# Kernel optimization log

Hardware: AMD Instinct MI355X
Metric: run time of the kernel (lower is better)

## Reference

```python
import jax, jax.numpy as jnp
import numpy as np

DIM_MODEL = 1024
NUM_HEADS = 16
HEAD_DIM = DIM_MODEL // NUM_HEADS
DIM_POS = 64
EVENT_HORIZON = 1e-06
MAX_FORCE = 50.0
CURVATURE = 0.15


def setup_inputs() -> dict:
    key = jax.random.key(0)
    k1, k2, k3, k4 = jax.random.split(key, 4)
    B, S = 2, 2048
    x = jax.random.normal(k1, (B, S, DIM_MODEL), dtype=jnp.float32)
    positions = jax.random.normal(k2, (S, DIM_POS), dtype=jnp.float32)
    # learned params
    W_mass = jax.random.normal(k3, (NUM_HEADS, HEAD_DIM), dtype=jnp.float32) * (1.0 / np.sqrt(HEAD_DIM))
    G = jnp.asarray([1.0 * 0.9 ** h for h in range(NUM_HEADS)], dtype=jnp.float32)
    W_out = jax.random.normal(k4, (DIM_MODEL, DIM_MODEL), dtype=jnp.float32) * (1.0 / np.sqrt(DIM_MODEL))
    return {"x": x, "positions": positions, "W_mass": W_mass, "G": G, "W_out": W_out}


def reference(x, positions, W_mass, G, W_out):
    B, S, D = x.shape
    H, hd = NUM_HEADS, HEAD_DIM
    xh = x.reshape(B, S, H, hd)                      # per-head slices (contiguous split)
    # per-head scalar "mass" per token: softplus(Linear(head_dim -> 1, no bias))
    masses = jax.nn.softplus(jnp.einsum('bshd,hd->bhs', xh, W_mass))  # [B,H,S]
    # shared squared distances between positions, with curvature warp
    diff = positions[None, :, :] - positions[:, None, :]  # [S,S,P]
    dist_sq = jnp.sum(diff * diff, axis=-1)               # [S,S]
    dist_norm = jnp.sqrt(dist_sq + EVENT_HORIZON)
    dist_sq = dist_sq * (1.0 + CURVATURE * jnp.cos(dist_norm))
    dist_sq = jnp.maximum(dist_sq, EVENT_HORIZON)
    # gravitational force scores F_ij = G * m_i * m_j / dist_sq, Hawking-clamped
    Gabs = jnp.abs(G)[None, :, None, None]                # [1,H,1,1]
    forces = Gabs * masses[:, :, :, None] * masses[:, :, None, :] / dist_sq[None, None]
    forces = jnp.minimum(forces, MAX_FORCE)               # [B,H,S,S]
    attn = jax.nn.softmax(forces, axis=-1)
    out = jnp.einsum('bhst,bthd->bshd', attn, xh).reshape(B, S, D)
    return out @ W_out.T
```

## Files before the change

### kernel.cpp

```cpp
#include <hip/hip_runtime.h>
#include <hip/hip_bf16.h>

#define SEQ 2048
#define DMODEL 1024
#define NHEAD 16
#define HDIM 64
#define DPOS 64
#define BATCH 2

constexpr float EVENT_HORIZON = 1e-6f;
constexpr float MAX_FORCE = 50.0f;
constexpr float CURV = 0.15f;
constexpr float LOG2E = 1.44269504f;
constexpr float SHIFT = 39.0f;

typedef __attribute__((ext_vector_type(8))) short frag8;
typedef __attribute__((ext_vector_type(4))) unsigned int uint4v;
typedef __attribute__((ext_vector_type(8))) _Float16 half8;
typedef __attribute__((ext_vector_type(2))) _Float16 half2t;
typedef __attribute__((ext_vector_type(4))) float frag4f;

union A8u { half8 v; half2t h[4]; };

__device__ inline short bfbits(float f) {
  __hip_bfloat16 h = __float2bfloat16(f);
  return *reinterpret_cast<short*>(&h);
}
__device__ inline float fbits(unsigned u) {
  union { unsigned u; float f; } c; c.u = u; return c.f;
}
__device__ inline half2t pkrtz(float a, float b) {
  return __builtin_bit_cast(half2t, __builtin_amdgcn_cvt_pkrtz(a, b));
}
__device__ inline float exp2_fast(float x) {
  float r;
  asm("v_exp_f32 %0, %1" : "=v"(r) : "v"(x));
  return r;
}
__device__ inline unsigned pkmax(unsigned a, unsigned b) {
  unsigned d;
  asm("v_pk_max_i16 %0, %1, %2" : "=v"(d) : "v"(a), "v"(b));
  return d;
}
__device__ inline int swz(int row, int u) { return row * 8 + (u ^ (row & 7)); }

__global__ __launch_bounds__(256) void prep_and_dist(
    const float* __restrict__ x, const float* __restrict__ Wm,
    const float* __restrict__ pos, const float* __restrict__ Wout,
    _Float16* __restrict__ xt, float* __restrict__ masses,
    unsigned short* __restrict__ invd, _Float16* __restrict__ wh) {
  __shared__ float Li[64 * 68];
  __shared__ float Lj[64 * 68];
  int bid = blockIdx.x;
  int t = threadIdx.x;

  if (bid >= 3072) {
    int i = (bid - 3072) * 256 + t;
    float4 v = ((const float4*)Wout)[i];
    _Float16 o[4] = {(_Float16)v.x, (_Float16)v.y, (_Float16)v.z, (_Float16)v.w};
    *(float2*)(wh + 4 * (size_t)i) = *(float2*)o;
    return;
  }

  if (bid < 2048) {
    int bh = bid & 31;
    int h = bh & 15, b = bh >> 4;
    int d = t & 63;
    int jg = (t >> 6) + ((bid >> 5) << 2);
    int j0 = jg * 8;
    const float* src = x + (size_t)(b * SEQ) * DMODEL + h * HDIM + d;
    float wmd = Wm[h * HDIM + d];
    half8 v;
    float fv[8];
#pragma unroll
    for (int jj = 0; jj < 8; ++jj) {
      float f = src[(size_t)(j0 + jj) * DMODEL];
      fv[jj] = f;
      v[jj] = (_Float16)f;
    }
    *(half8*)(xt + ((size_t)bh * HDIM + d) * SEQ + j0) = v;

    float msum = 0.f;
#pragma unroll
    for (int jj = 0; jj < 8; ++jj) {
      float s = fv[jj] * wmd;
#pragma unroll
      for (int off = 32; off; off >>= 1) s += __shfl_xor(s, off, 64);
      if (d == jj) msum = s;
    }
    if (d < 8) {
      float m = (msum > 20.f) ? msum : log1pf(expf(msum));
      masses[(size_t)bh * SEQ + j0 + d] = m;
    }
    return;
  }

  int ib = bid - 2048;
  int i0 = (ib >> 5) * 64, j0 = (ib & 31) * 64;
  if (i0 > j0) return;

  int kk = (t & 15) * 4;
  int rr = t >> 4;
#pragma unroll
  for (int q = 0; q < 4; ++q) {
    int row = q * 16 + rr;
    float4 a = *(const float4*)(pos + (size_t)(i0 + row) * DPOS + kk);
    float4 b = *(const float4*)(pos + (size_t)(j0 + row) * DPOS + kk);
    Li[(kk + 0) * 68 + row] = a.x; Li[(kk + 1) * 68 + row] = a.y;
    Li[(kk + 2) * 68 + row] = a.z; Li[(kk + 3) * 68 + row] = a.w;
    Lj[(kk + 0) * 68 + row] = b.x; Lj[(kk + 1) * 68 + row] = b.y;
    Lj[(kk + 2) * 68 + row] = b.z; Lj[(kk + 3) * 68 + row] = b.w;
  }
  __syncthreads();

  int ti = (t >> 4) * 4;
  int tj = (t & 15) * 4;

  float acc[4][4];
#pragma unroll
  for (int a = 0; a < 4; ++a)
#pragma unroll
    for (int b = 0; b < 4; ++b) acc[a][b] = 0.f;

#pragma unroll 8
  for (int k = 0; k < 64; ++k) {
    float4 a = *(const float4*)(&Li[k * 68 + ti]);
    float4 b = *(const float4*)(&Lj[k * 68 + tj]);
    float av[4] = {a.x, a.y, a.z, a.w};
    float bv[4] = {b.x, b.y, b.z, b.w};
#pragma unroll
    for (int mi = 0; mi < 4; ++mi)
#pragma unroll
      for (int mj = 0; mj < 4; ++mj) {
        float d = av[mi] - bv[mj];
        acc[mi][mj] += d * d;
      }
  }

  unsigned short op[4][4];
#pragma unroll
  for (int mi = 0; mi < 4; ++mi) {
#pragma unroll
    for (int mj = 0; mj < 4; ++mj) {
      float d2 = acc[mi][mj];
      float dn = sqrtf(d2 + EVENT_HORIZON);
      float wv = d2 * (1.f + CURV * __cosf(dn));
      op[mi][mj] = (unsigned short)bfbits(1.0f / fmaxf(wv, EVENT_HORIZON));
    }
    ushort4 o = {op[mi][0], op[mi][1], op[mi][2], op[mi][3]};
    *(ushort4*)(&invd[(size_t)(i0 + ti + mi) * SEQ + j0 + tj]) = o;
  }
#pragma unroll
  for (int mj = 0; mj < 4; ++mj) {
    ushort4 o = {op[0][mj], op[1][mj], op[2][mj], op[3][mj]};
    *(ushort4*)(&invd[(size_t)(j0 + tj + mj) * SEQ + i0 + ti]) = o;
  }
}

__global__ __launch_bounds__(256, 4) void attn_mfma_kernel(
    const _Float16* __restrict__ xt, const float* __restrict__ masses,
    const unsigned short* __restrict__ invd, const float* __restrict__ G,
    _Float16* __restrict__ attnout) {
  __shared__ _Float16 Vs[2][2][64 * 64];
  __shared__ float Ms[2][128];
  __shared__ float Mmax[16];

  constexpr float S2 = SHIFT * LOG2E;
  constexpr float C2 = (MAX_FORCE - SHIFT) * LOG2E;
  constexpr float THR = S2 - 26.f;

  int bid = blockIdx.x;
  int bh = (bid & 7) * 4 + ((bid >> 3) & 3);
  int iblk = bid >> 5;
  int h = bh & (NHEAD - 1), b = bh >> 4;
  int i0 = iblk * 64;
  int t = threadIdx.x, w = t >> 6, lane = t & 63;
  int l15 = lane & 15, quad = lane >> 4;
  int iw = i0 + w * 16;

  float gabs = fabsf(G[h]);
  const float* mrow = masses + (size_t)bh * SEQ;
  float cm = gabs * mrow[iw + l15] * LOG2E;
  const unsigned short* ivrow = invd + (size_t)(iw + l15) * SEQ;

  float cmx = cm;
#pragma unroll
  for (int off = 1; off < 16; off <<= 1) cmx = fmaxf(cmx, __shfl_xor(cmx, off, 64));

  int srow = t >> 2, sunit = (t & 3) * 2;
  const _Float16* srcrow =
      xt + ((size_t)bh * HDIM + srow) * SEQ + sunit * 8;
  int swzoff0 = swz(srow, sunit) * 8;
  int swzoff1 = swz(srow, sunit + 1) * 8;

  half8 vone;
#pragma unroll
  for (int k = 0; k < 8; ++k) vone[k] = (_Float16)1.f;

  frag4f acc[4];
#pragma unroll
  for (int nt = 0; nt < 4; ++nt) acc[nt] = (frag4f)0.f;
  frag4f accs = (frag4f)0.f;

  {
    const float* mp = mrow + t * 8;
    float4 q0 = *(const float4*)(mp);
    float4 q1 = *(const float4*)(mp + 4);
    float v0 = fmaxf(fmaxf(fmaxf(q0.x, q0.y), fmaxf(q0.z, q0.w)),
                     fmaxf(fmaxf(q1.x, q1.y), fmaxf(q1.z, q1.w)));
#pragma unroll
    for (int off = 1; off < 16; off <<= 1) v0 = fmaxf(v0, __shfl_xor(v0, off, 64));
    if ((t & 15) == 0) Mmax[t >> 4] = v0;
  }

  *(half8*)(&Vs[0][0][0] + swzoff0) = *(const half8*)(srcrow);
  *(half8*)(&Vs[0][0][0] + swzoff1) = *(const half8*)(srcrow + 8);
  *(half8*)(&Vs[0][1][0] + swzoff0) = *(const half8*)(srcrow + 64);
  *(half8*)(&Vs[0][1][0] + swzoff1) = *(const half8*)(srcrow + 72);
  if (t < 128) Ms[0][t] = mrow[t];
  frag8 iv_cur[4], iv_nxt[4];
  iv_cur[0] = *(const frag8*)(ivrow + quad * 8);
  iv_cur[1] = *(const frag8*)(ivrow + 32 + quad * 8);
  iv_cur[2] = *(const frag8*)(ivrow + 64 + quad * 8);
  iv_cur[3] = *(const frag8*)(ivrow + 96 + quad * 8);
  __syncthreads();

  for (int cc = 0; cc < 8; ++cc) {
#pragma unroll
    for (int u = 0; u < 2; ++u) {
      int c = cc * 2 + u;
      int jn = (c + 1) * 128;
      half8 vpre0, vpre1, vpre2, vpre3;
      float mload = 0.f;

      if (c < 15) {
        vpre0 = *(const half8*)(srcrow + jn);
        vpre1 = *(const half8*)(srcrow + jn + 8);
        if (t < 128) mload = mrow[jn + t];
        iv_nxt[0] = *(const frag8*)(ivrow + jn + quad * 8);
        iv_nxt[1] = *(const frag8*)(ivrow + jn + 32 + quad * 8);
      }

      bool live;
      {
        uint4v q0 = __builtin_bit_cast(uint4v, iv_cur[0]);
        uint4v q1 = __builtin_bit_cast(uint4v, iv_cur[1]);
        uint4v q2 = __builtin_bit_cast(uint4v, iv_cur[2]);
        uint4v q3 = __builtin_bit_cast(uint4v, iv_cur[3]);
        unsigned m0 = pkmax(pkmax(q0[0], q1[0]), pkmax(q2[0], q3[0]));
        unsigned m1 = pkmax(pkmax(q0[1], q1[1]), pkmax(q2[1], q3[1]));
        unsigned m2 = pkmax(pkmax(q0[2], q1[2]), pkmax(q2[2], q3[2]));
        unsigned m3 = pkmax(pkmax(q0[3], q1[3]), pkmax(q2[3], q3[3]));
        unsigned r = pkmax(pkmax(m0, m1), pkmax(m2, m3));
        float ivm = fmaxf(fbits(r << 16), fbits(r & 0xffff0000u));
#pragma unroll
        for (int off = 1; off < 64; off <<= 1)
          ivm = fmaxf(ivm, __shfl_xor(ivm, off, 64));
        live = (cmx * Mmax[c] * ivm >= THR);
      }

      const float* Mbase = &Ms[u][0];
      auto unit = [&](const _Float16* Vb, int sub, int kh, frag8 ivv) {
        const float* mp = Mbase + sub * 64 + kh * 32 + quad * 8;
        float4 mjl = *(const float4*)(mp);
        float4 mjh = *(const float4*)(mp + 4);
        float mjf[8] = {mjl.x, mjl.y, mjl.z, mjl.w,
                        mjh.x, mjh.y, mjh.z, mjh.w};
        uint4v uv = __builtin_bit_cast(uint4v, ivv);
        float e[8];
#pragma unroll
        for (int p = 0; p < 4; ++p) {
          float ivA = fbits(uv[p] << 16);
          float ivB = fbits(uv[p] & 0xffff0000u);
          float fA = fmaf(cm * mjf[2 * p], ivA, -S2);
          float fB = fmaf(cm * mjf[2 * p + 1], ivB, -S2);
          e[2 * p] = exp2_fast(fminf(fA, C2));
          e[2 * p + 1] = exp2_fast(fminf(fB, C2));
        }
        A8u A;
#pragma unroll
        for (int p = 0; p < 4; ++p)
          A.h[p] = pkrtz(e[2 * p], e[2 * p + 1]);

        __builtin_amdgcn_s_setprio(1);
        accs = __builtin_amdgcn_mfma_f32_16x16x32_f16(A.v, vone, accs, 0, 0, 0);
#pragma unroll
        for (int nt = 0; nt < 4; ++nt) {
          half8 Bf = *(const half8*)(Vb + swz(nt * 16 + l15, kh * 4 + quad) * 8);
          acc[nt] = __builtin_amdgcn_mfma_f32_16x16x32_f16(A.v, Bf, acc[nt], 0, 0, 0);
        }
        __builtin_amdgcn_s_setprio(0);
      };

      if (live) {
        unit(&Vs[u][0][0], 0, 0, iv_cur[0]);
        unit(&Vs[u][0][0], 0, 1, iv_cur[1]);
      }

      if (c < 15) {
        vpre2 = *(const half8*)(srcrow + jn + 64);
        vpre3 = *(const half8*)(srcrow + jn + 72);
        iv_nxt[2] = *(const frag8*)(ivrow + jn + 64 + quad * 8);
        iv_nxt[3] = *(const frag8*)(ivrow + jn + 96 + quad * 8);
      }

      if (live) {
        unit(&Vs[u][1][0], 1, 0, iv_cur[2]);
        unit(&Vs[u][1][0], 1, 1, iv_cur[3]);
      }

      if (c < 15) {
        _Float16* Vn = &Vs[u ^ 1][0][0];
        *(half8*)(Vn + swzoff0) = vpre0;
        *(half8*)(Vn + swzoff1) = vpre1;
        *(half8*)(Vn + 4096 + swzoff0) = vpre2;
        *(half8*)(Vn + 4096 + swzoff1) = vpre3;
        if (t < 128) Ms[u ^ 1][t] = mload;
        iv_cur[0] = iv_nxt[0]; iv_cur[1] = iv_nxt[1];
        iv_cur[2] = iv_nxt[2]; iv_cur[3] = iv_nxt[3];
      }
      __syncthreads();
    }
  }

#pragma unroll
  for (int reg = 0; reg < 4; ++reg) {
    int r = quad * 4 + reg;
    float s = 1.f / accs[reg];
#pragma unroll
    for (int nt = 0; nt < 4; ++nt) {
      attnout[(size_t)(b * SEQ + iw + r) * DMODEL + h * HDIM + nt * 16 + l15] =
          (_Float16)(acc[nt][reg] * s);
    }
  }
}

__global__ __launch_bounds__(512, 4) void out_gemm_mfma(
    const _Float16* __restrict__ Ag, const _Float16* __restrict__ Wg,
    float* __restrict__ C) {
  __shared__ _Float16 As[2][128 * 64];
  __shared__ _Float16 Bs[2][64 * 64];

  int bid = blockIdx.x;
  int xcd = bid & 7, local = bid >> 3;
  int m0 = (xcd * 4 + (local >> 4)) * 128;
  int n0 = (local & 15) * 64;

  int t = threadIdx.x, w = t >> 6, lane = t & 63;
  int l15 = lane & 15, quad = lane >> 4;
  int mh = (w >> 1) * 32, nh = (w & 1) * 32;

  int ar = t >> 2;  int au = (t & 3) * 2;
  int br = t >> 3;  int bu = t & 7;
  const _Float16* abase = Ag + (size_t)(m0 + ar) * DMODEL + au * 8;
  const _Float16* wbase = Wg + (size_t)(n0 + br) * DMODEL + bu * 8;

  frag4f acc[2][2];
#pragma unroll
  for (int mt = 0; mt < 2; ++mt)
#pragma unroll
    for (int nt = 0; nt < 2; ++nt) acc[mt][nt] = (frag4f)0.f;

  half8 a0, a1, b0;
  auto loadk = [&](int kc) {
    const _Float16* ap = abase + kc * 64;
    a0 = *(const half8*)(ap);
    a1 = *(const half8*)(ap + 8);
    b0 = *(const half8*)(wbase + kc * 64);
  };
  auto stage = [&](int buf) {
    _Float16* aw = As[buf]; _Float16* bw = Bs[buf];
    *(half8*)(aw + swz(ar, au + 0) * 8) = a0;
    *(half8*)(aw + swz(ar, au + 1) * 8) = a1;
    *(half8*)(bw + swz(br, bu) * 8) = b0;
  };

  loadk(0);
  stage(0);
  __syncthreads();

  for (int kk = 0; kk < 8; ++kk) {
#pragma unroll
    for (int u = 0; u < 2; ++u) {
      int kc = kk * 2 + u;
      if (kc < 15) loadk(kc + 1);

      const _Float16* ac = As[u];
      const _Float16* bc = Bs[u];
#pragma unroll
      for (int kh = 0; kh < 2; ++kh) {
        half8 Af[2], Bf[2];
#pragma unroll
        for (int mt = 0; mt < 2; ++mt)
          Af[mt] = *(const half8*)(ac + swz(mh + mt * 16 + l15, kh * 4 + quad) * 8);
#pragma unroll
        for (int nt = 0; nt < 2; ++nt)
          Bf[nt] = *(const half8*)(bc + swz(nh + nt * 16 + l15, kh * 4 + quad) * 8);
        __builtin_amdgcn_s_setprio(1);
#pragma unroll
        for (int mt = 0; mt < 2; ++mt)
#pragma unroll
          for (int nt = 0; nt < 2; ++nt)
            acc[mt][nt] = __builtin_amdgcn_mfma_f32_16x16x32_f16(Af[mt], Bf[nt], acc[mt][nt], 0, 0, 0);
        __builtin_amdgcn_s_setprio(0);
      }

      if (kc < 15) stage(u ^ 1);
      __syncthreads();
    }
  }

#pragma unroll
  for (int mt = 0; mt < 2; ++mt)
#pragma unroll
    for (int nt = 0; nt < 2; ++nt)
#pragma unroll
      for (int reg = 0; reg < 4; ++reg) {
        int m = m0 + mh + mt * 16 + quad * 4 + reg;
        int n = n0 + nh + nt * 16 + l15;
        C[(size_t)m * DMODEL + n] = acc[mt][nt][reg];
      }
}

extern "C" void kernel_launch(void* const* d_in, const int* in_sizes, int n_in,
                              void* d_out, int out_size, void* d_ws, size_t ws_size,
                              hipStream_t stream) {
  const float* x    = (const float*)d_in[0];
  const float* pos  = (const float*)d_in[1];
  const float* Wm   = (const float*)d_in[2];
  const float* G    = (const float*)d_in[3];
  const float* Wout = (const float*)d_in[4];
  float* out = (float*)d_out;

  char* wsb = (char*)d_ws;
  float* masses = (float*)wsb;
  unsigned short* invd = (unsigned short*)(wsb + (1 << 18));
  _Float16* attnout = (_Float16*)(wsb + (1 << 18) + (8 << 20));
  _Float16* xt      = (_Float16*)(wsb + (1 << 18) + (16 << 20));
  _Float16* wh      = (_Float16*)(wsb + (1 << 18) + (24 << 20));

  prep_and_dist<<<dim3(4096), 256, 0, stream>>>(
      x, Wm, pos, Wout, xt, masses, invd, wh);
  attn_mfma_kernel<<<dim3(1024), 256, 0, stream>>>(
      xt, masses, invd, G, attnout);
  out_gemm_mfma<<<dim3(512), 512, 0, stream>>>(attnout, wh, out);
}
```

Measured before the change: 150.7 us.

## Precompute per-tile inverse-distance maxima and skip loads for dead attention chunks

```diff
diff --git a/kernel.cpp b/kernel.cpp
--- a/kernel.cpp
+++ b/kernel.cpp
@@ -37,18 +37,14 @@
   asm("v_exp_f32 %0, %1" : "=v"(r) : "v"(x));
   return r;
 }
-__device__ inline unsigned pkmax(unsigned a, unsigned b) {
-  unsigned d;
-  asm("v_pk_max_i16 %0, %1, %2" : "=v"(d) : "v"(a), "v"(b));
-  return d;
-}
 __device__ inline int swz(int row, int u) { return row * 8 + (u ^ (row & 7)); }
 
 __global__ __launch_bounds__(256) void prep_and_dist(
     const float* __restrict__ x, const float* __restrict__ Wm,
     const float* __restrict__ pos, const float* __restrict__ Wout,
     _Float16* __restrict__ xt, float* __restrict__ masses,
-    unsigned short* __restrict__ invd, _Float16* __restrict__ wh) {
+    unsigned short* __restrict__ invd, _Float16* __restrict__ wh,
+    float* __restrict__ tilemax) {
   __shared__ float Li[64 * 68];
   __shared__ float Lj[64 * 68];
   int bid = blockIdx.x;
@@ -138,6 +134,7 @@
   }
 
   unsigned short op[4][4];
+  int mloc = 0;
 #pragma unroll
   for (int mi = 0; mi < 4; ++mi) {
 #pragma unroll
@@ -146,6 +143,7 @@
       float dn = sqrtf(d2 + EVENT_HORIZON);
       float wv = d2 * (1.f + CURV * __cosf(dn));
       op[mi][mj] = (unsigned short)bfbits(1.0f / fmaxf(wv, EVENT_HORIZON));
+      mloc = max(mloc, (int)op[mi][mj]);
     }
     ushort4 o = {op[mi][0], op[mi][1], op[mi][2], op[mi][3]};
     *(ushort4*)(&invd[(size_t)(i0 + ti + mi) * SEQ + j0 + tj]) = o;
@@ -155,15 +153,32 @@
     ushort4 o = {op[0][mj], op[1][mj], op[2][mj], op[3][mj]};
     *(ushort4*)(&invd[(size_t)(j0 + tj + mj) * SEQ + i0 + ti]) = o;
   }
+
+#pragma unroll
+  for (int off = 1; off < 64; off <<= 1)
+    mloc = max(mloc, __shfl_xor(mloc, off, 64));
+  __syncthreads();
+  if ((t & 63) == 0) ((int*)Li)[t >> 6] = mloc;
+  __syncthreads();
+  if (t == 0) {
+    int mm = max(max(((int*)Li)[0], ((int*)Li)[1]),
+                 max(((int*)Li)[2], ((int*)Li)[3]));
+    float fm = fbits((unsigned)mm << 16);
+    int it = ib >> 5, jt = ib & 31;
+    tilemax[it * 32 + jt] = fm;
+    tilemax[jt * 32 + it] = fm;
+  }
 }
 
 __global__ __launch_bounds__(256, 4) void attn_mfma_kernel(
     const _Float16* __restrict__ xt, const float* __restrict__ masses,
     const unsigned short* __restrict__ invd, const float* __restrict__ G,
-    _Float16* __restrict__ attnout) {
+    const float* __restrict__ tilemax, _Float16* __restrict__ attnout) {
   __shared__ _Float16 Vs[2][2][64 * 64];
   __shared__ float Ms[2][128];
   __shared__ float Mmax[16];
+  __shared__ float CMW[4];
+  __shared__ int Lv[16];
 
   constexpr float S2 = SHIFT * LOG2E;
   constexpr float C2 = (MAX_FORCE - SHIFT) * LOG2E;
@@ -183,10 +198,6 @@
   float cm = gabs * mrow[iw + l15] * LOG2E;
   const unsigned short* ivrow = invd + (size_t)(iw + l15) * SEQ;
 
-  float cmx = cm;
-#pragma unroll
-  for (int off = 1; off < 16; off <<= 1) cmx = fmaxf(cmx, __shfl_xor(cmx, off, 64));
-
   int srow = t >> 2, sunit = (t & 3) * 2;
   const _Float16* srcrow =
       xt + ((size_t)bh * HDIM + srow) * SEQ + sunit * 8;
@@ -211,6 +222,12 @@
 #pragma unroll
     for (int off = 1; off < 16; off <<= 1) v0 = fmaxf(v0, __shfl_xor(v0, off, 64));
     if ((t & 15) == 0) Mmax[t >> 4] = v0;
+  }
+  {
+    float cmx = cm;
+#pragma unroll
+    for (int off = 1; off < 16; off <<= 1) cmx = fmaxf(cmx, __shfl_xor(cmx, off, 64));
+    if (lane == 0) CMW[w] = cmx;
   }
 
   *(half8*)(&Vs[0][0][0] + swzoff0) = *(const half8*)(srcrow);
@@ -225,38 +242,34 @@
   iv_cur[3] = *(const frag8*)(ivrow + 96 + quad * 8);
   __syncthreads();
 
+  if (t < 16) {
+    float cmb = fmaxf(fmaxf(CMW[0], CMW[1]), fmaxf(CMW[2], CMW[3]));
+    float ivm = fmaxf(tilemax[iblk * 32 + 2 * t], tilemax[iblk * 32 + 2 * t + 1]);
+    Lv[t] = (cmb * Mmax[t] * ivm >= THR) ? 1 : 0;
+  }
+  __syncthreads();
+  unsigned livemask = 0;
+#pragma unroll
+  for (int c2 = 0; c2 < 16; ++c2)
+    livemask |= (unsigned)(Lv[c2] != 0) << c2;
+  livemask = __builtin_amdgcn_readfirstlane(livemask);
+
   for (int cc = 0; cc < 8; ++cc) {
 #pragma unroll
     for (int u = 0; u < 2; ++u) {
       int c = cc * 2 + u;
       int jn = (c + 1) * 128;
+      bool lvc = (livemask >> c) & 1;
+      bool lvn = (c < 15) && ((livemask >> (c + 1)) & 1);
       half8 vpre0, vpre1, vpre2, vpre3;
       float mload = 0.f;
 
-      if (c < 15) {
+      if (lvn) {
         vpre0 = *(const half8*)(srcrow + jn);
         vpre1 = *(const half8*)(srcrow + jn + 8);
         if (t < 128) mload = mrow[jn + t];
         iv_nxt[0] = *(const frag8*)(ivrow + jn + quad * 8);
         iv_nxt[1] = *(const frag8*)(ivrow + jn + 32 + quad * 8);
-      }
-
-      bool live;
-      {
-        uint4v q0 = __builtin_bit_cast(uint4v, iv_cur[0]);
-        uint4v q1 = __builtin_bit_cast(uint4v, iv_cur[1]);
-        uint4v q2 = __builtin_bit_cast(uint4v, iv_cur[2]);
-        uint4v q3 = __builtin_bit_cast(uint4v, iv_cur[3]);
-        unsigned m0 = pkmax(pkmax(q0[0], q1[0]), pkmax(q2[0], q3[0]));
-        unsigned m1 = pkmax(pkmax(q0[1], q1[1]), pkmax(q2[1], q3[1]));
-        unsigned m2 = pkmax(pkmax(q0[2], q1[2]), pkmax(q2[2], q3[2]));
-        unsigned m3 = pkmax(pkmax(q0[3], q1[3]), pkmax(q2[3], q3[3]));
-        unsigned r = pkmax(pkmax(m0, m1), pkmax(m2, m3));
-        float ivm = fmaxf(fbits(r << 16), fbits(r & 0xffff0000u));
-#pragma unroll
-        for (int off = 1; off < 64; off <<= 1)
-          ivm = fmaxf(ivm, __shfl_xor(ivm, off, 64));
-        live = (cmx * Mmax[c] * ivm >= THR);
       }
 
       const float* Mbase = &Ms[u][0];
@@ -292,24 +305,24 @@
         __builtin_amdgcn_s_setprio(0);
       };
 
-      if (live) {
+      if (lvc) {
         unit(&Vs[u][0][0], 0, 0, iv_cur[0]);
         unit(&Vs[u][0][0], 0, 1, iv_cur[1]);
       }
 
-      if (c < 15) {
+      if (lvn) {
         vpre2 = *(const half8*)(srcrow + jn + 64);
         vpre3 = *(const half8*)(srcrow + jn + 72);
         iv_nxt[2] = *(const frag8*)(ivrow + jn + 64 + quad * 8);
         iv_nxt[3] = *(const frag8*)(ivrow + jn + 96 + quad * 8);
       }
 
-      if (live) {
+      if (lvc) {
         unit(&Vs[u][1][0], 1, 0, iv_cur[2]);
         unit(&Vs[u][1][0], 1, 1, iv_cur[3]);
       }
 
-      if (c < 15) {
+      if (lvn) {
         _Float16* Vn = &Vs[u ^ 1][0][0];
         *(half8*)(Vn + swzoff0) = vpre0;
         *(half8*)(Vn + swzoff1) = vpre1;
@@ -326,7 +339,7 @@
 #pragma unroll
   for (int reg = 0; reg < 4; ++reg) {
     int r = quad * 4 + reg;
-    float s = 1.f / accs[reg];
+    float s = (accs[reg] > 0.f) ? (1.f / accs[reg]) : 0.f;
 #pragma unroll
     for (int nt = 0; nt < 4; ++nt) {
       attnout[(size_t)(b * SEQ + iw + r) * DMODEL + h * HDIM + nt * 16 + l15] =
@@ -438,10 +451,11 @@
   _Float16* attnout = (_Float16*)(wsb + (1 << 18) + (8 << 20));
   _Float16* xt      = (_Float16*)(wsb + (1 << 18) + (16 << 20));
   _Float16* wh      = (_Float16*)(wsb + (1 << 18) + (24 << 20));
+  float* tilemax    = (float*)(wsb + (1 << 18) + (26 << 20));
 
   prep_and_dist<<<dim3(4096), 256, 0, stream>>>(
-      x, Wm, pos, Wout, xt, masses, invd, wh);
+      x, Wm, pos, Wout, xt, masses, invd, wh, tilemax);
   attn_mfma_kernel<<<dim3(1024), 256, 0, stream>>>(
-      xt, masses, invd, G, attnout);
+      xt, masses, invd, G, tilemax, attnout);
   out_gemm_mfma<<<dim3(512), 512, 0, stream>>>(attnout, wh, out);
 }
```

New measurement: 121.9 us. -19.1%, faster.
